# Optimization experiments

Hardware: AMD Instinct MI355X
Metric: run time of the kernel (lower is better)

Reference implementation:

```python
import jax, jax.numpy as jnp
import numpy as np

PS = 4          # patch_size (square)
STRIDE = 2
PAD = (PS - 1) // 2
HEADS = 8
DIM = 256       # attn_dim == dim (kv_dim > dim, dim_reduc=1)
KV_DIM = 512
HD = DIM // HEADS
SCALE = HD ** -0.5
NP2 = PS * PS   # 16 elements per window


def _unfold(x, k, s, p):
    """torch.nn.functional.unfold: (B,C,H,W) -> (B, C*k*k, Ho*Wo)."""
    B, C, H, W = x.shape
    xp = jnp.pad(x, ((0, 0), (0, 0), (p, p), (p, p)))
    Ho = (H + 2 * p - k) // s + 1
    Wo = (W + 2 * p - k) // s + 1
    r = (jnp.arange(Ho) * s)[:, None] + jnp.arange(k)   # (Ho,k)
    c = (jnp.arange(Wo) * s)[:, None] + jnp.arange(k)   # (Wo,k)
    pt = xp[:, :, r][:, :, :, :, c]                     # (B,C,Ho,k,Wo,k)
    pt = pt.transpose(0, 1, 3, 5, 2, 4)                 # (B,C,k,k,Ho,Wo)
    return pt.reshape(B, C * k * k, Ho * Wo)


def _fold(y, C, Hout, Wout, k, s, p):
    """torch.nn.functional.fold: (B, C*k*k, Ho*Wo) -> (B,C,Hout,Wout), overlap-add."""
    B = y.shape[0]
    Ho = (Hout + 2 * p - k) // s + 1
    Wo = (Wout + 2 * p - k) // s + 1
    pt = y.reshape(B, C, k, k, Ho, Wo).transpose(0, 1, 4, 2, 5, 3)  # (B,C,Ho,k,Wo,k)
    r = (jnp.arange(Ho) * s)[:, None] + jnp.arange(k)
    c = (jnp.arange(Wo) * s)[:, None] + jnp.arange(k)
    out = jnp.zeros((B, C, Hout + 2 * p, Wout + 2 * p), y.dtype)
    out = out.at[:, :, r[:, :, None, None], c[None, None, :, :]].add(pt)
    return out[:, :, p:Hout + p, p:Wout + p]


def _patch_softmax(attn, Ht, Wt, Hb, Wb):
    """Normalize exp(attn) by per-bottom-pixel sums computed via a fold/unfold round trip
    (faithful to the original, including its reshape layout)."""
    a = jnp.exp(attn)                                                # (B*HtWt, H, 16, 1)
    s = a.reshape(-1, Ht * Wt, HEADS, NP2).transpose(0, 2, 3, 1)     # (B, H, 16, HtWt)
    s = s.reshape(-1, NP2, Ht * Wt)                                  # (B*H, 16, HtWt)
    s = _fold(s, 1, Hb, Wb, PS, STRIDE, PAD)                         # (B*H, 1, Hb, Wb)
    s = _unfold(s, PS, STRIDE, PAD).transpose(0, 2, 1)               # (B*H, HtWt, 16)
    s = jnp.where(s == 0, jnp.ones((), s.dtype), s)
    return a / s.reshape(-1, HEADS, NP2, 1)


def _forward(Xt, Xb, q_w, kv_w, proj_w, proj_b, rel_init, rel_bias, Ht, Wt, Hb, Wb):
    B, _, C = Xb.shape
    # im2col: gather 4x4 windows of the fine map, one window per coarse token
    Xbp = Xb.transpose(0, 2, 1).reshape(B, C, Hb, Wb)
    Xbp = _unfold(Xbp, PS, STRIDE, PAD)                              # (B, C*16, Ht*Wt)
    Xbp = Xbp.reshape(B, C, NP2, Ht * Wt).transpose(0, 3, 2, 1)
    Xbp = Xbp.reshape(B * Ht * Wt, NP2, C)                           # queries (top_down)
    Xtq = Xt.reshape(-1, 1, Xt.shape[-1])                            # (B*HtWt, 1, kv_dim)

    q = (Xbp @ q_w.T).reshape(-1, NP2, HEADS, HD).transpose(0, 2, 1, 3)  # (BHW,H,16,hd)
    kv = (Xtq @ kv_w.T).reshape(-1, 1, 2, HEADS, HD).transpose(2, 0, 3, 1, 4)
    k, v = kv[0], kv[1]                                              # (BHW,H,1,hd)

    attn = (q @ jnp.swapaxes(k, -2, -1)) * SCALE                     # (BHW,H,16,1)
    attn = attn + rel_init[:, None] + rel_bias[:, None]
    attn = _patch_softmax(attn, Ht, Wt, Hb, Wb)

    out = (attn @ v).transpose(0, 2, 1, 3).reshape(-1, NP2, DIM)     # (BHW,16,DIM)
    out = out.reshape(B, Ht * Wt, NP2, DIM).transpose(0, 3, 2, 1)
    out = out.reshape(B, DIM * NP2, Ht * Wt)
    out = _fold(out, DIM, Hb, Wb, PS, STRIDE, PAD)                   # (B,DIM,Hb,Wb)
    out = out.transpose(0, 2, 3, 1).reshape(B, Hb * Wb, DIM)
    return out @ proj_w.T + proj_b


def setup_inputs() -> dict:
    key = jax.random.key(0)
    ks = jax.random.split(key, 7)
    B, Ht, Wt, Hb, Wb = 4, 64, 64, 128, 128
    return {
        "Xt": jax.random.normal(ks[0], (B, Ht * Wt, KV_DIM), jnp.float32),
        "Xb": jax.random.normal(ks[1], (B, Hb * Wb, DIM), jnp.float32),
        "q_w": jax.random.normal(ks[2], (DIM, DIM), jnp.float32) * 0.02,
        "kv_w": jax.random.normal(ks[3], (2 * DIM, KV_DIM), jnp.float32) * 0.02,
        "proj_w": jax.random.normal(ks[4], (DIM, DIM), jnp.float32) * 0.02,
        "proj_b": jnp.zeros((DIM,), jnp.float32),
        "rel_init": jax.random.normal(ks[5], (NP2,), jnp.float32) * 0.02,
        "rel_bias": jax.random.normal(ks[6], (NP2,), jnp.float32) * 0.02,
        "Ht": Ht, "Wt": Wt, "Hb": Hb, "Wb": Wb,
    }


def reference(Xt, Xb, q_w, kv_w, proj_w, proj_b, rel_init, rel_bias, Ht, Wt, Hb, Wb):
    return _forward(Xt, Xb, q_w, kv_w, proj_w, proj_b, rel_init, rel_bias, Ht, Wt, Hb, Wb)
```

## Files before the change

kernel.cpp:

```cpp
#include <hip/hip_runtime.h>
#include <math.h>

constexpr int B_    = 4;
constexpr int HT    = 64,  WT = 64;
constexpr int HB    = 128, WB = 128;
constexpr int DIM   = 256;
constexpr int KVD   = 512;
constexpr int HEADS = 8;
constexpr int NP2   = 16;
constexpr int NPIX  = HB * WB;
constexpr int NWIN  = HT * WT;
constexpr float SCALE = 0.17677669529663687f;

using bf16x8 = __attribute__((ext_vector_type(8))) short;
using f32x4  = __attribute__((ext_vector_type(4))) float;

__device__ __forceinline__ unsigned short f2bf(float f) {
  union { float f; unsigned u; } v; v.f = f;
  unsigned r = v.u + 0x7fffu + ((v.u >> 16) & 1u);
  return (unsigned short)(r >> 16);
}
__device__ __forceinline__ unsigned pack_bf16(float x, float y) {
  unsigned ux = __float_as_uint(x) + 0x8000u;
  unsigned uy = __float_as_uint(y) + 0x8000u;
  return __builtin_amdgcn_perm(uy, ux, 0x07060302u);
}

constexpr int NXT4  = B_ * NWIN * KVD / 4;
constexpr int NQW4  = DIM * DIM / 4;
constexpr int NKVW4 = KVD * KVD / 4;
constexpr int NCAST4 = NXT4 + NQW4 + NKVW4 + NQW4;

__global__ __launch_bounds__(256) void cast_all(
    const float* __restrict__ Xt, const float* __restrict__ qw,
    const float* __restrict__ kvw, const float* __restrict__ pw,
    unsigned short* __restrict__ Xth, unsigned short* __restrict__ qwh,
    unsigned short* __restrict__ kvwh, unsigned short* __restrict__ pwh)
{
  const int i = blockIdx.x * 256 + threadIdx.x;
  const float* src; unsigned short* dst; int off;
  if (i < NXT4)                     { src = Xt;  dst = Xth;  off = i; }
  else if (i < NXT4 + NQW4)         { src = qw;  dst = qwh;  off = i - NXT4; }
  else if (i < NXT4 + NQW4 + NKVW4) { src = kvw; dst = kvwh; off = i - NXT4 - NQW4; }
  else                              { src = pw;  dst = pwh;  off = i - NXT4 - NQW4 - NKVW4; }
  float4 v = ((const float4*)src)[off];
  ushort4 o;
  o.x = f2bf(v.x); o.y = f2bf(v.y); o.z = f2bf(v.z); o.w = f2bf(v.w);
  ((ushort4*)dst)[off] = o;
}

template<bool AF32, int BN, bool BF16_OUT, bool BIAS>
__device__ __forceinline__ void gemm_core(
    const void* __restrict__ Ap, const unsigned short* __restrict__ Bw,
    const float* __restrict__ bias, void* __restrict__ Cp,
    int M, int N, int K, int bx, int by,
    unsigned short* Ash, unsigned short* Bsh)
{
  constexpr int NT = BN / 32;
  const int tid  = threadIdx.x;
  const int wave = tid >> 6;
  const int lane = tid & 63;
  const int m0 = bx * 128;
  const int n0 = by * BN;
  const int wm = (wave >> 1) * 64;
  const int wn = (wave & 1) * (BN / 2);

  f32x4 acc[4][NT];
#pragma unroll
  for (int i = 0; i < 4; ++i)
#pragma unroll
    for (int j = 0; j < NT; ++j) { f32x4 z = {0.f, 0.f, 0.f, 0.f}; acc[i][j] = z; }

  const float* Af = (const float*)Ap;
  float4 areg[4];
  auto loadA = [&](int kk) {
#pragma unroll
    for (int u = 0; u < 4; ++u) {
      const int c = u * 256 + tid, row = c >> 3, kq = (c & 7) * 4;
      areg[u] = *(const float4*)(Af + (size_t)(m0 + row) * K + kk + kq);
    }
  };
  if constexpr (AF32) loadA(0);

  const int fr = lane & 15;
  const int fk = (lane >> 4) * 8;

  for (int kk = 0; kk < K; kk += 32) {
    __syncthreads();
    if constexpr (AF32) {
#pragma unroll
      for (int u = 0; u < 4; ++u) {
        const int c = u * 256 + tid, row = c >> 3, kq = (c & 7) * 4;
        uint2 pk;
        pk.x = pack_bf16(areg[u].x, areg[u].y);
        pk.y = pack_bf16(areg[u].z, areg[u].w);
        *(uint2*)&Ash[row * 32 + kq] = pk;
      }
    } else {
      const unsigned short* Ab = (const unsigned short*)Ap;
#pragma unroll
      for (int i = 0; i < 2; ++i) {
        const int c = i * 256 + wave * 64 + lane, row = c >> 2, ko = (c & 3) * 8;
        __builtin_amdgcn_global_load_lds(
            (const __attribute__((address_space(1))) unsigned int*)
                (Ab + (size_t)(m0 + row) * K + kk + ko),
            (__attribute__((address_space(3))) unsigned int*)
                ((char*)Ash + i * 4096 + wave * 1024),
            16, 0, 0);
      }
    }
#pragma unroll
    for (int i = 0; i < BN / 64; ++i) {
      const int c = i * 256 + wave * 64 + lane, row = c >> 2, ko = (c & 3) * 8;
      __builtin_amdgcn_global_load_lds(
          (const __attribute__((address_space(1))) unsigned int*)
              (Bw + (size_t)(n0 + row) * K + kk + ko),
          (__attribute__((address_space(3))) unsigned int*)
              ((char*)Bsh + i * 4096 + wave * 1024),
          16, 0, 0);
    }
    __syncthreads();

    if constexpr (AF32) { if (kk + 32 < K) loadA(kk + 32); }

    bf16x8 af[4], bf[NT];
#pragma unroll
    for (int t = 0; t < 4; ++t)
      af[t] = *(const bf16x8*)&Ash[(wm + t * 16 + fr) * 32 + fk];
#pragma unroll
    for (int t = 0; t < NT; ++t)
      bf[t] = *(const bf16x8*)&Bsh[(wn + t * 16 + fr) * 32 + fk];
#pragma unroll
    for (int mt = 0; mt < 4; ++mt)
#pragma unroll
      for (int nt = 0; nt < NT; ++nt)
        acc[mt][nt] = __builtin_amdgcn_mfma_f32_16x16x32_bf16(
            af[mt], bf[nt], acc[mt][nt], 0, 0, 0);
  }

  const int col0 = lane & 15;
  const int rb   = (lane >> 4) * 4;
#pragma unroll
  for (int mt = 0; mt < 4; ++mt)
#pragma unroll
    for (int nt = 0; nt < NT; ++nt) {
      const int col = n0 + wn + nt * 16 + col0;
      float bv = BIAS ? bias[col] : 0.f;
#pragma unroll
      for (int r = 0; r < 4; ++r) {
        const int row = m0 + wm + mt * 16 + rb + r;
        const float v = acc[mt][nt][r] + bv;
        if (BF16_OUT) ((unsigned short*)Cp)[(size_t)row * N + col] = f2bf(v);
        else          ((float*)Cp)[(size_t)row * N + col] = v;
      }
    }
}

__global__ __launch_bounds__(256, 2) void g12_kernel(
    const float* __restrict__ Xb, const unsigned short* __restrict__ qwh,
    unsigned short* __restrict__ Qh,
    const unsigned short* __restrict__ Xth, const unsigned short* __restrict__ kvwh,
    unsigned short* __restrict__ KVh)
{
  __shared__ unsigned short Ash[128 * 32];
  __shared__ unsigned short Bsh[256 * 32];
  const int id = blockIdx.x;
  if ((id & 1) == 0) {
    gemm_core<true, 256, true, false>(Xb, qwh, nullptr, Qh,
        B_ * NPIX, DIM, DIM, id >> 1, 0, Ash, Bsh);
  } else {
    const int t = id >> 1;
    gemm_core<false, 128, true, false>(Xth, kvwh, nullptr, KVh,
        B_ * NWIN, KVD, KVD, t >> 2, t & 3, Ash, Bsh);
  }
}

__global__ __launch_bounds__(256, 2) void g3_kernel(
    const unsigned short* __restrict__ Oh, const unsigned short* __restrict__ pwh,
    const float* __restrict__ pb, float* __restrict__ out)
{
  __shared__ unsigned short Ash[128 * 32];
  __shared__ unsigned short Bsh[256 * 32];
  gemm_core<false, 256, false, true>(Oh, pwh, pb, out,
      B_ * NPIX, DIM, DIM, blockIdx.x, 0, Ash, Bsh);
}

__global__ __launch_bounds__(256) void es_kernel(
    const unsigned short* __restrict__ Qh, const unsigned short* __restrict__ KVh,
    const float* __restrict__ rel_init, const float* __restrict__ rel_bias,
    float* __restrict__ E, float* __restrict__ S)
{
  const int idx = blockIdx.x * 256 + threadIdx.x;
  const int h = idx & 7;
  const int x = (idx >> 3) & 127;
  const int y = (idx >> 10) & 127;
  const int b = idx >> 17;

  const uint4* qp = (const uint4*)(Qh + ((size_t)((b << 14) + y * WB + x)) * DIM + h * 32);
  uint4 q0 = qp[0], q1 = qp[1], q2 = qp[2], q3 = qp[3];
  const unsigned qa[16] = {q0.x,q0.y,q0.z,q0.w, q1.x,q1.y,q1.z,q1.w,
                           q2.x,q2.y,q2.z,q2.w, q3.x,q3.y,q3.z,q3.w};

  const int ilo = max(0, (y - 1) >> 1), ihi = min(HT - 1, (y + 1) >> 1);
  const int jlo = max(0, (x - 1) >> 1), jhi = min(WT - 1, (x + 1) >> 1);

  float s = 0.f;
  for (int i = ilo; i <= ihi; ++i)
    for (int j = jlo; j <= jhi; ++j) {
      const int w = i * WT + j;
      const int p = (y + 1 - 2 * i) * 4 + (x + 1 - 2 * j);
      const uint4* kp = (const uint4*)(KVh + ((size_t)((b << 12) + w)) * KVD + h * 32);
      uint4 k0 = kp[0], k1 = kp[1], k2 = kp[2], k3 = kp[3];
      const unsigned ka[16] = {k0.x,k0.y,k0.z,k0.w, k1.x,k1.y,k1.z,k1.w,
                               k2.x,k2.y,k2.z,k2.w, k3.x,k3.y,k3.z,k3.w};
      float acc = 0.f;
#pragma unroll
      for (int q = 0; q < 16; ++q) {
        acc = fmaf(__uint_as_float(qa[q] << 16),
                   __uint_as_float(ka[q] << 16), acc);
        acc = fmaf(__uint_as_float(qa[q] & 0xffff0000u),
                   __uint_as_float(ka[q] & 0xffff0000u), acc);
      }
      const float e = expf(acc * SCALE + rel_init[p] + rel_bias[p]);
      E[((size_t)((b << 12) + w)) * 128 + h * NP2 + p] = e;
      s += e;
    }
  S[(size_t)((b * HEADS + h) << 14) + y * WB + x] = s;
}

__global__ __launch_bounds__(256) void r_kernel(
    const float* __restrict__ E, const float* __restrict__ S,
    float* __restrict__ R)
{
  const int idx = blockIdx.x * 256 + threadIdx.x;
  const int b  = idx >> 19;
  const int r  = idx & 524287;
  const int w  = r >> 7;
  const int t7 = r & 127;
  const int h  = t7 >> 4, p = t7 & 15;

  const int h_eff = w >> 9;
  const int w_eff = ((w & 511) << 3) + h;
  const int i2 = w_eff >> 6, j2 = w_eff & 63;
  const int y2 = 2 * i2 + (p >> 2) - 1;
  const int x2 = 2 * j2 + (p & 3) - 1;
  float s = 1.f;
  if ((unsigned)y2 < (unsigned)HB && (unsigned)x2 < (unsigned)WB)
    s = S[(size_t)((b * HEADS + h_eff) * NPIX) + y2 * WB + x2];
  R[idx] = E[idx] / s;
}

__global__ __launch_bounds__(256) void o_kernel(
    const float* __restrict__ R, const unsigned short* __restrict__ KVh,
    unsigned short* __restrict__ out_pre)
{
  const int t  = threadIdx.x;
  const int pg = blockIdx.x * 8 + (t >> 5);
  const int b  = pg >> 14;
  const int yx = pg & 16383;
  const int y  = yx >> 7, x = yx & 127;
  const int c8 = t & 31;
  const int h  = c8 >> 2;

  const int ilo = max(0, (y - 1) >> 1), ihi = min(HT - 1, (y + 1) >> 1);
  const int jlo = max(0, (x - 1) >> 1), jhi = min(WT - 1, (x + 1) >> 1);

  float acc[8] = {};
  for (int i = ilo; i <= ihi; ++i)
    for (int j = jlo; j <= jhi; ++j) {
      const int w = i * WT + j;
      const int p = (y + 1 - 2 * i) * 4 + (x + 1 - 2 * j);
      const float rr = R[((size_t)(b * NWIN + w)) * 128 + h * NP2 + p];
      const uint4 v = *(const uint4*)(KVh + ((size_t)(b * NWIN + w)) * KVD + 256 + c8 * 8);
      const unsigned vv[4] = {v.x, v.y, v.z, v.w};
#pragma unroll
      for (int q = 0; q < 4; ++q) {
        acc[2*q]   = fmaf(rr, __uint_as_float(vv[q] << 16),         acc[2*q]);
        acc[2*q+1] = fmaf(rr, __uint_as_float(vv[q] & 0xffff0000u), acc[2*q+1]);
      }
    }

  uint4 ov;
  ov.x = (unsigned)f2bf(acc[0]) | ((unsigned)f2bf(acc[1]) << 16);
  ov.y = (unsigned)f2bf(acc[2]) | ((unsigned)f2bf(acc[3]) << 16);
  ov.z = (unsigned)f2bf(acc[4]) | ((unsigned)f2bf(acc[5]) << 16);
  ov.w = (unsigned)f2bf(acc[6]) | ((unsigned)f2bf(acc[7]) << 16);
  *(uint4*)(out_pre + (size_t)pg * DIM + c8 * 8) = ov;
}

extern "C" void kernel_launch(void* const* d_in, const int* in_sizes, int n_in,
                              void* d_out, int out_size, void* d_ws, size_t ws_size,
                              hipStream_t stream) {
  const float* Xt       = (const float*)d_in[0];
  const float* Xb       = (const float*)d_in[1];
  const float* q_w      = (const float*)d_in[2];
  const float* kv_w     = (const float*)d_in[3];
  const float* proj_w   = (const float*)d_in[4];
  const float* proj_b   = (const float*)d_in[5];
  const float* rel_init = (const float*)d_in[6];
  const float* rel_bias = (const float*)d_in[7];
  float* out = (float*)d_out;

  char* ws = (char*)d_ws;
  const size_t nXb = (size_t)B_ * NPIX * DIM;
  const size_t nXt = (size_t)B_ * NWIN * KVD;
  const size_t nQW = (size_t)DIM * DIM;
  const size_t nKVW = (size_t)KVD * KVD;
  unsigned short* Qh   = (unsigned short*)ws;  ws += nXb * 2;
  unsigned short* Xth  = (unsigned short*)ws;  ws += nXt * 2;
  unsigned short* KVh  = (unsigned short*)ws;  ws += nXt * 2;
  float*          E    = (float*)ws;           ws += (size_t)B_ * NWIN * 128 * 4;
  float*          S    = (float*)ws;           ws += (size_t)B_ * HEADS * NPIX * 4;
  unsigned short* qwh  = (unsigned short*)ws;  ws += nQW * 2;
  unsigned short* kvwh = (unsigned short*)ws;  ws += nKVW * 2;
  unsigned short* pwh  = (unsigned short*)ws;  ws += nQW * 2;
  float*          R    = (float*)Xth;
  unsigned short* Oh   = Qh;

  const dim3 blk(256);

  cast_all<<<dim3(NCAST4 / 256), blk, 0, stream>>>(
      Xt, q_w, kv_w, proj_w, Xth, qwh, kvwh, pwh);

  g12_kernel<<<dim3(1024), blk, 0, stream>>>(Xb, qwh, Qh, Xth, kvwh, KVh);

  es_kernel<<<dim3(B_ * NPIX * HEADS / 256), blk, 0, stream>>>(
      Qh, KVh, rel_init, rel_bias, E, S);

  r_kernel<<<dim3(B_ * NWIN * 128 / 256), blk, 0, stream>>>(E, S, R);

  o_kernel<<<dim3(B_ * NPIX / 8), blk, 0, stream>>>(R, KVh, Oh);

  g3_kernel<<<dim3(B_ * NPIX / 128), blk, 0, stream>>>(Oh, pwh, proj_b, out);
}
```

Before: 253.2 us.

## Rewrite GEMMs as register-direct MFMA, fuse Xt cast and softmax normalize

```diff
diff --git a/kernel.cpp b/kernel.cpp
--- a/kernel.cpp
+++ b/kernel.cpp
@@ -25,164 +25,164 @@
   unsigned uy = __float_as_uint(y) + 0x8000u;
   return __builtin_amdgcn_perm(uy, ux, 0x07060302u);
 }
-
-constexpr int NXT4  = B_ * NWIN * KVD / 4;
+__device__ __forceinline__ bf16x8 pack8(const float4 x, const float4 y) {
+  union { unsigned u[4]; bf16x8 v; } r;
+  r.u[0] = pack_bf16(x.x, x.y);
+  r.u[1] = pack_bf16(x.z, x.w);
+  r.u[2] = pack_bf16(y.x, y.y);
+  r.u[3] = pack_bf16(y.z, y.w);
+  return r.v;
+}
+
 constexpr int NQW4  = DIM * DIM / 4;
 constexpr int NKVW4 = KVD * KVD / 4;
-constexpr int NCAST4 = NXT4 + NQW4 + NKVW4 + NQW4;
-
-__global__ __launch_bounds__(256) void cast_all(
-    const float* __restrict__ Xt, const float* __restrict__ qw,
-    const float* __restrict__ kvw, const float* __restrict__ pw,
-    unsigned short* __restrict__ Xth, unsigned short* __restrict__ qwh,
-    unsigned short* __restrict__ kvwh, unsigned short* __restrict__ pwh)
+constexpr int NCW4  = NQW4 + NKVW4 + NQW4;
+
+__global__ __launch_bounds__(256) void cast_w(
+    const float* __restrict__ qw, const float* __restrict__ kvw,
+    const float* __restrict__ pw,
+    unsigned short* __restrict__ qwh, unsigned short* __restrict__ kvwh,
+    unsigned short* __restrict__ pwh)
 {
   const int i = blockIdx.x * 256 + threadIdx.x;
   const float* src; unsigned short* dst; int off;
-  if (i < NXT4)                     { src = Xt;  dst = Xth;  off = i; }
-  else if (i < NXT4 + NQW4)         { src = qw;  dst = qwh;  off = i - NXT4; }
-  else if (i < NXT4 + NQW4 + NKVW4) { src = kvw; dst = kvwh; off = i - NXT4 - NQW4; }
-  else                              { src = pw;  dst = pwh;  off = i - NXT4 - NQW4 - NKVW4; }
+  if (i < NQW4)              { src = qw;  dst = qwh;  off = i; }
+  else if (i < NQW4 + NKVW4) { src = kvw; dst = kvwh; off = i - NQW4; }
+  else                       { src = pw;  dst = pwh;  off = i - NQW4 - NKVW4; }
   float4 v = ((const float4*)src)[off];
   ushort4 o;
   o.x = f2bf(v.x); o.y = f2bf(v.y); o.z = f2bf(v.z); o.w = f2bf(v.w);
   ((ushort4*)dst)[off] = o;
 }
 
-template<bool AF32, int BN, bool BF16_OUT, bool BIAS>
-__device__ __forceinline__ void gemm_core(
+template<bool AF32, int AD, int KC, int NC, int MT, bool BF16_OUT, bool BIAS>
+__device__ __forceinline__ void rgemm(
     const void* __restrict__ Ap, const unsigned short* __restrict__ Bw,
     const float* __restrict__ bias, void* __restrict__ Cp,
-    int M, int N, int K, int bx, int by,
-    unsigned short* Ash, unsigned short* Bsh)
-{
-  constexpr int NT = BN / 32;
-  const int tid  = threadIdx.x;
-  const int wave = tid >> 6;
-  const int lane = tid & 63;
-  const int m0 = bx * 128;
-  const int n0 = by * BN;
-  const int wm = (wave >> 1) * 64;
-  const int wn = (wave & 1) * (BN / 2);
-
-  f32x4 acc[4][NT];
-#pragma unroll
-  for (int i = 0; i < 4; ++i)
-#pragma unroll
-    for (int j = 0; j < NT; ++j) { f32x4 z = {0.f, 0.f, 0.f, 0.f}; acc[i][j] = z; }
-
-  const float* Af = (const float*)Ap;
-  float4 areg[4];
-  auto loadA = [&](int kk) {
-#pragma unroll
-    for (int u = 0; u < 4; ++u) {
-      const int c = u * 256 + tid, row = c >> 3, kq = (c & 7) * 4;
-      areg[u] = *(const float4*)(Af + (size_t)(m0 + row) * K + kk + kq);
-    }
-  };
-  if constexpr (AF32) loadA(0);
-
+    const int m0, const int n0)
+{
+  constexpr int KS = KC / 32;
+  constexpr int U  = MT * KS;
+  const int lane = threadIdx.x & 63;
   const int fr = lane & 15;
   const int fk = (lane >> 4) * 8;
 
-  for (int kk = 0; kk < K; kk += 32) {
-    __syncthreads();
-    if constexpr (AF32) {
-#pragma unroll
-      for (int u = 0; u < 4; ++u) {
-        const int c = u * 256 + tid, row = c >> 3, kq = (c & 7) * 4;
-        uint2 pk;
-        pk.x = pack_bf16(areg[u].x, areg[u].y);
-        pk.y = pack_bf16(areg[u].z, areg[u].w);
-        *(uint2*)&Ash[row * 32 + kq] = pk;
+  const unsigned short* __restrict__ Ab = (const unsigned short*)Ap;
+  const float* __restrict__          Af = (const float*)Ap;
+
+  f32x4 acc[4][4];
+#pragma unroll
+  for (int i = 0; i < 4; ++i)
+#pragma unroll
+    for (int j = 0; j < 4; ++j) { f32x4 z = {0.f,0.f,0.f,0.f}; acc[i][j] = z; }
+
+  bf16x8 a16[AF32 ? 1 : AD][4];
+  float4 a32[AF32 ? AD : 1][4][2];
+  bf16x8 b16[2][4];
+
+  auto loadA = [&](int u, int buf) {
+    const int ar = m0 + (u / KS) * 128;
+    const int ko = (u % KS) * 32 + fk;
+#pragma unroll
+    for (int t = 0; t < 4; ++t) {
+      const size_t ao = (size_t)(ar + t * 16 + fr) * KC + ko;
+      if constexpr (AF32) {
+        a32[buf][t][0] = *(const float4*)(Af + ao);
+        a32[buf][t][1] = *(const float4*)(Af + ao + 4);
+      } else {
+        a16[buf][t] = *(const bf16x8*)(Ab + ao);
       }
-    } else {
-      const unsigned short* Ab = (const unsigned short*)Ap;
-#pragma unroll
-      for (int i = 0; i < 2; ++i) {
-        const int c = i * 256 + wave * 64 + lane, row = c >> 2, ko = (c & 3) * 8;
-        __builtin_amdgcn_global_load_lds(
-            (const __attribute__((address_space(1))) unsigned int*)
-                (Ab + (size_t)(m0 + row) * K + kk + ko),
-            (__attribute__((address_space(3))) unsigned int*)
-                ((char*)Ash + i * 4096 + wave * 1024),
-            16, 0, 0);
-      }
-    }
-#pragma unroll
-    for (int i = 0; i < BN / 64; ++i) {
-      const int c = i * 256 + wave * 64 + lane, row = c >> 2, ko = (c & 3) * 8;
-      __builtin_amdgcn_global_load_lds(
-          (const __attribute__((address_space(1))) unsigned int*)
-              (Bw + (size_t)(n0 + row) * K + kk + ko),
-          (__attribute__((address_space(3))) unsigned int*)
-              ((char*)Bsh + i * 4096 + wave * 1024),
-          16, 0, 0);
-    }
-    __syncthreads();
-
-    if constexpr (AF32) { if (kk + 32 < K) loadA(kk + 32); }
-
-    bf16x8 af[4], bf[NT];
+    }
+  };
+  auto loadB = [&](int u, int buf) {
+    const int ko = (u % KS) * 32 + fk;
 #pragma unroll
     for (int t = 0; t < 4; ++t)
-      af[t] = *(const bf16x8*)&Ash[(wm + t * 16 + fr) * 32 + fk];
-#pragma unroll
-    for (int t = 0; t < NT; ++t)
-      bf[t] = *(const bf16x8*)&Bsh[(wn + t * 16 + fr) * 32 + fk];
+      b16[buf][t] = *(const bf16x8*)(Bw + (size_t)(n0 + t * 16 + fr) * KC + ko);
+  };
+
+#pragma unroll
+  for (int d = 0; d < AD; ++d) loadA(d, d);
+  loadB(0, 0);
+  loadB(1, 1);
+
+#pragma unroll
+  for (int u = 0; u < U; ++u) {
+    const int ab = u % AD;
+    const int bb = u & 1;
+    bf16x8 af[4];
+#pragma unroll
+    for (int t = 0; t < 4; ++t) {
+      if constexpr (AF32) af[t] = pack8(a32[ab][t][0], a32[ab][t][1]);
+      else                af[t] = a16[ab][t];
+    }
+    __builtin_amdgcn_s_setprio(1);
 #pragma unroll
     for (int mt = 0; mt < 4; ++mt)
 #pragma unroll
-      for (int nt = 0; nt < NT; ++nt)
+      for (int nt = 0; nt < 4; ++nt)
         acc[mt][nt] = __builtin_amdgcn_mfma_f32_16x16x32_bf16(
-            af[mt], bf[nt], acc[mt][nt], 0, 0, 0);
+            af[mt], b16[bb][nt], acc[mt][nt], 0, 0, 0);
+    __builtin_amdgcn_s_setprio(0);
+    if (u + AD < U) loadA(u + AD, ab);
+    if (u + 2  < U) loadB(u + 2, bb);
+
+    if (((u + 1) % KS) == 0) {
+      const int mb = m0 + (u / KS) * 128;
+      const int col0 = lane & 15, rb = (lane >> 4) * 4;
+#pragma unroll
+      for (int mt = 0; mt < 4; ++mt)
+#pragma unroll
+        for (int nt = 0; nt < 4; ++nt) {
+          const int col = n0 + nt * 16 + col0;
+          const float bv = BIAS ? bias[col] : 0.f;
+#pragma unroll
+          for (int r = 0; r < 4; ++r) {
+            const int row = mb + mt * 16 + rb + r;
+            const float v = acc[mt][nt][r] + bv;
+            if constexpr (BF16_OUT)
+              ((unsigned short*)Cp)[(size_t)row * NC + col] = f2bf(v);
+            else
+              ((float*)Cp)[(size_t)row * NC + col] = v;
+          }
+          if constexpr (MT > 1) { f32x4 z = {0.f,0.f,0.f,0.f}; acc[mt][nt] = z; }
+        }
+    }
   }
-
-  const int col0 = lane & 15;
-  const int rb   = (lane >> 4) * 4;
-#pragma unroll
-  for (int mt = 0; mt < 4; ++mt)
-#pragma unroll
-    for (int nt = 0; nt < NT; ++nt) {
-      const int col = n0 + wn + nt * 16 + col0;
-      float bv = BIAS ? bias[col] : 0.f;
-#pragma unroll
-      for (int r = 0; r < 4; ++r) {
-        const int row = m0 + wm + mt * 16 + rb + r;
-        const float v = acc[mt][nt][r] + bv;
-        if (BF16_OUT) ((unsigned short*)Cp)[(size_t)row * N + col] = f2bf(v);
-        else          ((float*)Cp)[(size_t)row * N + col] = v;
-      }
-    }
 }
 
 __global__ __launch_bounds__(256, 2) void g12_kernel(
     const float* __restrict__ Xb, const unsigned short* __restrict__ qwh,
     unsigned short* __restrict__ Qh,
-    const unsigned short* __restrict__ Xth, const unsigned short* __restrict__ kvwh,
+    const float* __restrict__ Xt, const unsigned short* __restrict__ kvwh,
     unsigned short* __restrict__ KVh)
 {
-  __shared__ unsigned short Ash[128 * 32];
-  __shared__ unsigned short Bsh[256 * 32];
+  const int wave = threadIdx.x >> 6;
+  const int wr = wave >> 1, wc = wave & 1;
   const int id = blockIdx.x;
-  if ((id & 1) == 0) {
-    gemm_core<true, 256, true, false>(Xb, qwh, nullptr, Qh,
-        B_ * NPIX, DIM, DIM, id >> 1, 0, Ash, Bsh);
+  const int g = id >> 3, r = id & 7;
+  const int i = (g >> 1) * 8 + r;
+  if ((g & 1) == 0) {
+    const int bx = i >> 1, by = i & 1;
+    rgemm<true, 3, 256, 256, 2, true, false>(
+        Xb, qwh, nullptr, Qh, bx * 256 + wr * 64, by * 128 + wc * 64);
   } else {
-    const int t = id >> 1;
-    gemm_core<false, 128, true, false>(Xth, kvwh, nullptr, KVh,
-        B_ * NWIN, KVD, KVD, t >> 2, t & 3, Ash, Bsh);
+    const int bx = i >> 2, by = i & 3;
+    rgemm<true, 3, 512, 512, 1, true, false>(
+        Xt, kvwh, nullptr, KVh, bx * 128 + wr * 64, by * 128 + wc * 64);
   }
 }
 
-__global__ __launch_bounds__(256, 2) void g3_kernel(
+__global__ __launch_bounds__(256) void g3_kernel(
     const unsigned short* __restrict__ Oh, const unsigned short* __restrict__ pwh,
     const float* __restrict__ pb, float* __restrict__ out)
 {
-  __shared__ unsigned short Ash[128 * 32];
-  __shared__ unsigned short Bsh[256 * 32];
-  gemm_core<false, 256, false, true>(Oh, pwh, pb, out,
-      B_ * NPIX, DIM, DIM, blockIdx.x, 0, Ash, Bsh);
+  const int wave = threadIdx.x >> 6;
+  const int wr = wave >> 1, wc = wave & 1;
+  const int id = blockIdx.x;
+  const int bx = id >> 1, by = id & 1;
+  rgemm<false, 2, 256, 256, 2, false, true>(
+      Oh, pwh, pb, out, bx * 256 + wr * 64, by * 128 + wc * 64);
 }
 
 __global__ __launch_bounds__(256) void es_kernel(
@@ -228,30 +228,9 @@
   S[(size_t)((b * HEADS + h) << 14) + y * WB + x] = s;
 }
 
-__global__ __launch_bounds__(256) void r_kernel(
+__global__ __launch_bounds__(256) void o_kernel(
     const float* __restrict__ E, const float* __restrict__ S,
-    float* __restrict__ R)
-{
-  const int idx = blockIdx.x * 256 + threadIdx.x;
-  const int b  = idx >> 19;
-  const int r  = idx & 524287;
-  const int w  = r >> 7;
-  const int t7 = r & 127;
-  const int h  = t7 >> 4, p = t7 & 15;
-
-  const int h_eff = w >> 9;
-  const int w_eff = ((w & 511) << 3) + h;
-  const int i2 = w_eff >> 6, j2 = w_eff & 63;
-  const int y2 = 2 * i2 + (p >> 2) - 1;
-  const int x2 = 2 * j2 + (p & 3) - 1;
-  float s = 1.f;
-  if ((unsigned)y2 < (unsigned)HB && (unsigned)x2 < (unsigned)WB)
-    s = S[(size_t)((b * HEADS + h_eff) * NPIX) + y2 * WB + x2];
-  R[idx] = E[idx] / s;
-}
-
-__global__ __launch_bounds__(256) void o_kernel(
-    const float* __restrict__ R, const unsigned short* __restrict__ KVh,
+    const unsigned short* __restrict__ KVh,
     unsigned short* __restrict__ out_pre)
 {
   const int t  = threadIdx.x;
@@ -270,7 +249,17 @@
     for (int j = jlo; j <= jhi; ++j) {
       const int w = i * WT + j;
       const int p = (y + 1 - 2 * i) * 4 + (x + 1 - 2 * j);
-      const float rr = R[((size_t)(b * NWIN + w)) * 128 + h * NP2 + p];
+      const float e = E[((size_t)((b << 12) + w)) * 128 + h * NP2 + p];
+      const int h_eff = w >> 9;
+      const int w_eff = ((w & 511) << 3) + h;
+      const int i2 = w_eff >> 6, j2 = w_eff & 63;
+      const int y2 = 2 * i2 + (p >> 2) - 1;
+      const int x2 = 2 * j2 + (p & 3) - 1;
+      float sd = 1.f;
+      if ((unsigned)y2 < (unsigned)HB && (unsigned)x2 < (unsigned)WB)
+        sd = S[(size_t)((b * HEADS + h_eff) * NPIX) + y2 * WB + x2];
+      const float rr = e / sd;
+
       const uint4 v = *(const uint4*)(KVh + ((size_t)(b * NWIN + w)) * KVD + 256 + c8 * 8);
       const unsigned vv[4] = {v.x, v.y, v.z, v.w};
 #pragma unroll
@@ -307,29 +296,25 @@
   const size_t nQW = (size_t)DIM * DIM;
   const size_t nKVW = (size_t)KVD * KVD;
   unsigned short* Qh   = (unsigned short*)ws;  ws += nXb * 2;
-  unsigned short* Xth  = (unsigned short*)ws;  ws += nXt * 2;
   unsigned short* KVh  = (unsigned short*)ws;  ws += nXt * 2;
   float*          E    = (float*)ws;           ws += (size_t)B_ * NWIN * 128 * 4;
   float*          S    = (float*)ws;           ws += (size_t)B_ * HEADS * NPIX * 4;
   unsigned short* qwh  = (unsigned short*)ws;  ws += nQW * 2;
   unsigned short* kvwh = (unsigned short*)ws;  ws += nKVW * 2;
   unsigned short* pwh  = (unsigned short*)ws;  ws += nQW * 2;
-  float*          R    = (float*)Xth;
   unsigned short* Oh   = Qh;
 
   const dim3 blk(256);
 
-  cast_all<<<dim3(NCAST4 / 256), blk, 0, stream>>>(
-      Xt, q_w, kv_w, proj_w, Xth, qwh, kvwh, pwh);
-
-  g12_kernel<<<dim3(1024), blk, 0, stream>>>(Xb, qwh, Qh, Xth, kvwh, KVh);
+  cast_w<<<dim3(NCW4 / 256), blk, 0, stream>>>(
+      q_w, kv_w, proj_w, qwh, kvwh, pwh);
+
+  g12_kernel<<<dim3(1024), blk, 0, stream>>>(Xb, qwh, Qh, Xt, kvwh, KVh);
 
   es_kernel<<<dim3(B_ * NPIX * HEADS / 256), blk, 0, stream>>>(
       Qh, KVh, rel_init, rel_bias, E, S);
 
-  r_kernel<<<dim3(B_ * NWIN * 128 / 256), blk, 0, stream>>>(E, S, R);
-
-  o_kernel<<<dim3(B_ * NPIX / 8), blk, 0, stream>>>(R, KVh, Oh);
+  o_kernel<<<dim3(B_ * NPIX / 8), blk, 0, stream>>>(E, S, KVh, Oh);
 
   g3_kernel<<<dim3(B_ * NPIX / 128), blk, 0, stream>>>(Oh, pwh, proj_b, out);
 }
```

After: 313.3 us. 23.7% more time.
